# Performance work log

Hardware: AMD Instinct MI355X
Metric: run time of the kernel (lower is better)

## Reference

```python
import jax, jax.numpy as jnp
import numpy as np

T_LEN, S_LEN, B = 100, 400, 16
D_IN, H, CTX, V = 512, 512, 1024, 50000


def setup_inputs() -> dict:
    key = jax.random.key(0)
    ks = jax.random.split(key, 16)
    p = lambda k, shp: jax.random.normal(k, shp, dtype=jnp.float32) * 0.05
    return {
        "y_emb": p(ks[0], (T_LEN, B, D_IN)),
        "context": p(ks[1], (S_LEN, B, CTX)),
        "init_h": p(ks[2], (B, H)),
        "init_c": p(ks[3], (B, H)),
        "x_mask": jnp.ones((S_LEN, B, 1), jnp.float32),
        "y_mask": jnp.ones((T_LEN, B, 1), jnp.float32),
        "y_idx": jax.random.randint(ks[4], (T_LEN, B), 0, V),
        # LSTMCell params (PyTorch gate order i,f,g,o)
        "W_ih": p(ks[5], (4 * H, D_IN)),
        "W_hh": p(ks[6], (4 * H, H)),
        "b_ih": jnp.zeros((4 * H,), jnp.float32),
        "b_hh": jnp.zeros((4 * H,), jnp.float32),
        # second gate block (order i,f,o,c per chunk names x4i,x4f,x4o,x4c)
        "Wx": p(ks[7], (4 * H, CTX)),
        "Ux": p(ks[8], (4 * H, H)),
        "bx": jnp.zeros((4 * H,), jnp.float32),
        # attention params
        "Wc_att": p(ks[9], (CTX, CTX)),
        "b_att": jnp.zeros((CTX,), jnp.float32),
        "W_comb_att": p(ks[10], (CTX, 2 * H)),
        "U_att": p(ks[11], (1, CTX)),
        # word prob: softmax(Linear(cat[h2, att, y_emb]))
        "Wp": p(ks[12], (V, H + CTX + D_IN)),
        "bp": jnp.zeros((V,), jnp.float32),
    }


def reference(y_emb, context, init_h, init_c, x_mask, y_mask, y_idx,
              W_ih, W_hh, b_ih, b_hh, Wx, Ux, bx,
              Wc_att, b_att, W_comb_att, U_att, Wp, bp):
    # pctx: [S, B, CTX]
    pctx = jnp.einsum('sbc,dc->sbd', context, Wc_att) + b_att
    u_att = U_att[0]  # [CTX]

    def step(carry, inp):
        h, c = carry              # [B, H] each
        y, ym, yi = inp           # [B, D_IN], [B, 1], [B]
        # LSTMCell (gate order i, f, g, o)
        gates = y @ W_ih.T + b_ih + h @ W_hh.T + b_hh
        gi, gf, gg, go = jnp.split(gates, 4, axis=1)
        c1 = jax.nn.sigmoid(gf) * c + jax.nn.sigmoid(gi) * jnp.tanh(gg)
        h1 = jax.nn.sigmoid(go) * jnp.tanh(c1)
        h1 = ym * h1 + (1.0 - ym) * h
        c1 = ym * c1 + (1.0 - ym) * c
        # attention query from cat(h1, c1)
        s = jnp.concatenate([h1, c1], axis=1)          # [B, 2H]
        q = s @ W_comb_att.T                           # [B, CTX]
        unreg = jnp.tanh(pctx + q) * x_mask            # [S, B, CTX]
        u = jnp.einsum('sbc,c->sb', unreg, u_att)[..., None]  # [S, B, 1]
        w = jnp.exp(u - jnp.max(u, axis=0, keepdims=True)) * x_mask
        w = w / jnp.sum(w, axis=0, keepdims=True)      # [S, B, 1]
        att = jnp.sum(w * context, axis=0)             # [B, CTX]
        # second gate block (chunk order i, f, o, c)
        pre = h1 @ Ux.T + att @ Wx.T + bx
        xi, xf, xo, xc = jnp.split(pre, 4, axis=1)
        c2 = jax.nn.sigmoid(xf) * c1 + jax.nn.sigmoid(xi) * jnp.tanh(xc)
        h2 = jax.nn.sigmoid(xo) * jnp.tanh(c2)
        c2 = ym * c2 + (1.0 - ym) * c1
        h2 = ym * h2 + (1.0 - ym) * h1
        # word prob + per-step NLL
        feat = jnp.concatenate([h2, att, y], axis=1)   # [B, H+CTX+D_IN]
        logp = jax.nn.log_softmax(feat @ Wp.T + bp, axis=1)
        cost = -jnp.take_along_axis(logp, yi[:, None], axis=1)[:, 0]  # [B]
        return (h2, c2), cost

    _, costs = jax.lax.scan(step, (init_h, init_c), (y_emb, y_mask, y_idx))
    ym2 = y_mask[..., 0]                               # [T, B]
    cost_per_batch = jnp.sum(costs * ym2, axis=0) / jnp.sum(ym2, axis=0)
    return cost_per_batch
```

## Files before the change

### kernel.cpp

```cpp
#include <hip/hip_runtime.h>
#include <stdint.h>

typedef unsigned int u32;
typedef unsigned short u16;
typedef unsigned char u8;
typedef long long i64;
typedef __attribute__((ext_vector_type(4))) float f32x4;
typedef __attribute__((ext_vector_type(4))) float f32x4v;
typedef __attribute__((ext_vector_type(8))) short bf16x8;

#define T_LEN 100
#define S_LEN 400
#define NB 16
#define HD 512
#define CTXD 1024
#define VOC 50000
#define K4H 2048
#define M_ALL 1600

static __device__ __forceinline__ float bf2f(u16 v) {
  union { u32 u; float f; } c; c.u = ((u32)v) << 16; return c.f;
}
static __device__ __forceinline__ u16 f2bf(float f) {
  union { float f; u32 u; } c; c.f = f;
  return (u16)((c.u + 0x7fffu + ((c.u >> 16) & 1u)) >> 16);
}
static __device__ __forceinline__ u32 pack2(float a, float b) {
  return (u32)f2bf(a) | ((u32)f2bf(b) << 16);
}
static __device__ __forceinline__ uint4 pack8(float4 a, float4 b) {
  return make_uint4(pack2(a.x, a.y), pack2(a.z, a.w), pack2(b.x, b.y), pack2(b.z, b.w));
}
static __device__ __forceinline__ uint4 pack8v(f32x4v a, f32x4v b) {
  return make_uint4(pack2(a.x, a.y), pack2(a.z, a.w), pack2(b.x, b.y), pack2(b.z, b.w));
}
static __device__ __forceinline__ u32 pkfp8(float x, float y, float z, float w) {
  int p = 0;
  p = __builtin_amdgcn_cvt_pk_fp8_f32(x, y, p, 0);
  p = __builtin_amdgcn_cvt_pk_fp8_f32(z, w, p, 1);
  return (u32)p;
}
static __device__ __forceinline__ float sigm(float x) { return 1.f / (1.f + __expf(-x)); }
static __device__ __forceinline__ float tanh_(float x) {
  float e = __expf(2.f * x);
  return 1.f - 2.f / (e + 1.f);
}
static __device__ __forceinline__ float ald(const float* p) {
  return __hip_atomic_load(p, __ATOMIC_RELAXED, __HIP_MEMORY_SCOPE_AGENT);
}
static __device__ __forceinline__ void ast(float* p, float v) {
  __hip_atomic_store(p, v, __ATOMIC_RELAXED, __HIP_MEMORY_SCOPE_AGENT);
}
static __device__ __forceinline__ f32x4v cld4(const float* p) {
  f32x4v v;
  asm volatile("global_load_dwordx4 %0, %1, off sc0 sc1\n\t"
               "s_waitcnt vmcnt(0)"
               : "=&v"(v) : "v"(p) : "memory");
  return v;
}
static __device__ __forceinline__ void cld8(
    const float* p0, const float* p1, const float* p2, const float* p3,
    const float* p4, const float* p5, const float* p6, const float* p7,
    f32x4v& v0, f32x4v& v1, f32x4v& v2, f32x4v& v3,
    f32x4v& v4, f32x4v& v5, f32x4v& v6, f32x4v& v7) {
  asm volatile(
      "global_load_dwordx4 %0, %8, off sc0 sc1\n\t"
      "global_load_dwordx4 %1, %9, off sc0 sc1\n\t"
      "global_load_dwordx4 %2, %10, off sc0 sc1\n\t"
      "global_load_dwordx4 %3, %11, off sc0 sc1\n\t"
      "global_load_dwordx4 %4, %12, off sc0 sc1\n\t"
      "global_load_dwordx4 %5, %13, off sc0 sc1\n\t"
      "global_load_dwordx4 %6, %14, off sc0 sc1\n\t"
      "global_load_dwordx4 %7, %15, off sc0 sc1\n\t"
      "s_waitcnt vmcnt(0)"
      : "=&v"(v0), "=&v"(v1), "=&v"(v2), "=&v"(v3),
        "=&v"(v4), "=&v"(v5), "=&v"(v6), "=&v"(v7)
      : "v"(p0), "v"(p1), "v"(p2), "v"(p3), "v"(p4), "v"(p5), "v"(p6), "v"(p7)
      : "memory");
}
static __device__ __forceinline__ void sig(u32* ctr) {
  __hip_atomic_fetch_add(ctr, 1u, __ATOMIC_RELAXED, __HIP_MEMORY_SCOPE_AGENT);
}
static __device__ __forceinline__ void waitge(u32* ctr, u32 tgt) {
  while (__hip_atomic_load(ctr, __ATOMIC_RELAXED, __HIP_MEMORY_SCOPE_AGENT) < tgt)
    __builtin_amdgcn_s_sleep(1);
}

__global__ void sentinel_kernel(float* out, float v) {
  if (threadIdx.x < NB) out[threadIdx.x] = v;
}

struct CastArgs {
  const float* src[9];
  u16* dst[9];
  u32 cum[10];
};

__global__ __launch_bounds__(256) void cast_all(CastArgs A) {
  u32 i = blockIdx.x * 256 + threadIdx.x;
  if (i >= A.cum[9]) return;
  int seg = 0;
  while (i >= A.cum[seg + 1]) seg++;
  u32 li = i - A.cum[seg];
  const float* s = A.src[seg];
  f32x4v a = __builtin_nontemporal_load((const f32x4v*)&s[li * 8]);
  f32x4v b = __builtin_nontemporal_load((const f32x4v*)&s[li * 8 + 4]);
  if (seg < 8) {
    *(uint4*)&A.dst[seg][li * 8] = pack8v(a, b);
  } else {
    u32 m = li >> 6, k8 = (li & 63) << 3;
    u8* f8 = (u8*)A.dst[8];
    uint2 t;
    t.x = pkfp8(a.x, a.y, a.z, a.w);
    t.y = pkfp8(b.x, b.y, b.z, b.w);
    *(uint2*)&f8[(size_t)m * K4H + 1536 + k8] = t;
  }
}

template <int MODE>
__global__ __launch_bounds__(256) void gemm_bf16(const u16* __restrict__ A,
                                                 const u16* __restrict__ Bw,
                                                 void* __restrict__ out,
                                                 const float* __restrict__ bias1,
                                                 const float* __restrict__ bias2,
                                                 int M, int N, int K) {
  __shared__ u16 As[64][40];
  __shared__ u16 Bs[64][40];
  int nb = N / 64;
  int m0 = (blockIdx.x / nb) * 64;
  int n0 = (blockIdx.x % nb) * 64;
  int tid = threadIdx.x;
  int lane = tid & 63;
  int w = tid >> 6;
  int wm = (w >> 1) * 32, wn = (w & 1) * 32;
  f32x4 acc[2][2] = {};
  int arow = tid >> 2, achk = (tid & 3) * 8;
  for (int k0 = 0; k0 < K; k0 += 32) {
    __syncthreads();
    *(uint4*)&As[arow][achk] = *(const uint4*)&A[(size_t)(m0 + arow) * K + k0 + achk];
    *(uint4*)&Bs[arow][achk] = *(const uint4*)&Bw[(size_t)(n0 + arow) * K + k0 + achk];
    __syncthreads();
    int r = lane & 15, kg = lane >> 4;
    bf16x8 a0 = *(const bf16x8*)&As[wm + r][kg * 8];
    bf16x8 a1 = *(const bf16x8*)&As[wm + 16 + r][kg * 8];
    bf16x8 b0 = *(const bf16x8*)&Bs[wn + r][kg * 8];
    bf16x8 b1 = *(const bf16x8*)&Bs[wn + 16 + r][kg * 8];
    acc[0][0] = __builtin_amdgcn_mfma_f32_16x16x32_bf16(a0, b0, acc[0][0], 0, 0, 0);
    acc[0][1] = __builtin_amdgcn_mfma_f32_16x16x32_bf16(a0, b1, acc[0][1], 0, 0, 0);
    acc[1][0] = __builtin_amdgcn_mfma_f32_16x16x32_bf16(a1, b0, acc[1][0], 0, 0, 0);
    acc[1][1] = __builtin_amdgcn_mfma_f32_16x16x32_bf16(a1, b1, acc[1][1], 0, 0, 0);
  }
  int col = lane & 15, rg = lane >> 4;
#pragma unroll
  for (int fi = 0; fi < 2; fi++)
#pragma unroll
    for (int fj = 0; fj < 2; fj++)
#pragma unroll
      for (int r = 0; r < 4; r++) {
        int m = m0 + wm + fi * 16 + rg * 4 + r;
        int n = n0 + wn + fj * 16 + col;
        float v = acc[fi][fj][r] + bias1[n];
        if constexpr (MODE == 1) {
          v += bias2[n];
          ((float*)out)[(size_t)m * N + n] = v;
        } else {
          ((u16*)out)[(size_t)m * N + n] = f2bf(v);
        }
      }
}

struct DecArgs {
  const u16 *pctx, *ctx, *Whh, *Wcomb, *Uxw, *Wxw;
  const float *xW, *bx, *uatt, *xmask, *ymask, *init_h, *init_c;
  float *h, *c, *h1, *c1, *qsum, *attnum, *attden;
  u8* feat8;
  u32* bar;
};

__global__ __launch_bounds__(256, 1) void decoder_coop(DecArgs A) {
  extern __shared__ char smem[];
  u16* pctx_l = (u16*)smem;
  u16* ctx_l = (u16*)(smem + 51200);
  float* ua_lp = (float*)(smem + 102400);
  float* xm_l = (float*)(smem + 106752);
  char* un = smem + 106880;

  const int tid = threadIdx.x;
  const int blk = blockIdx.x;
  const int lane = tid & 63, w = tid >> 6;
  const int r16 = lane & 15, kg = lane >> 4;
  const int bK = blk & 15;
  const int s0 = (blk >> 4) * 25;
  u32* qdone = A.bar;
  u32* cdone = A.bar + 64;
  u32* h2done = A.bar + 128;

  for (int idx = tid; idx < 25 * 128; idx += 256) {
    int i = idx >> 7, c8 = (idx & 127) << 3;
    *(uint4*)&pctx_l[i * 1024 + c8] =
        *(const uint4*)&A.pctx[((size_t)(s0 + i) * NB + bK) * CTXD + c8];
    *(uint4*)&ctx_l[i * 1024 + c8] =
        *(const uint4*)&A.ctx[((size_t)(s0 + i) * NB + bK) * CTXD + c8];
  }
  {
    int c0 = tid * 4;
    int p = (c0 >> 4) * 17 + (c0 & 15);
#pragma unroll
    for (int j = 0; j < 4; j++) ua_lp[p + j] = A.uatt[c0 + j];
  }
  if (tid < 25) xm_l[tid] = A.xmask[(s0 + tid) * NB + bK];

  for (int ts = 0; ts < T_LEN; ts++) {
    const int par = ts & 1;
    if (blk < 16) {
      if (tid == 0) waitge(h2done, 32u * (u32)ts);
      __syncthreads();
      u16* Al = (u16*)un;
      float* gbA = (float*)(un + 16640);
      u16* h1c1 = (u16*)(un + 24832);
      const float* hs = ts ? A.h : A.init_h;
      const float* cs = ts ? A.c : A.init_c;
      {
        const int b0_ = tid >> 6, k80 = (tid & 63) << 3;
        const int b1_ = (256 + tid) >> 6, k81 = ((256 + tid) & 63) << 3;
        const int b2_ = (512 + tid) >> 6, k82 = ((512 + tid) & 63) << 3;
        const int b3_ = (768 + tid) >> 6, k83 = ((768 + tid) & 63) << 3;
        f32x4v v0, v1, v2, v3, v4, v5, v6, v7;
        cld8(&hs[b0_ * 512 + k80], &hs[b0_ * 512 + k80 + 4],
             &hs[b1_ * 512 + k81], &hs[b1_ * 512 + k81 + 4],
             &hs[b2_ * 512 + k82], &hs[b2_ * 512 + k82 + 4],
             &hs[b3_ * 512 + k83], &hs[b3_ * 512 + k83 + 4],
             v0, v1, v2, v3, v4, v5, v6, v7);
        *(uint4*)&Al[b0_ * 520 + k80] = pack8v(v0, v1);
        *(uint4*)&Al[b1_ * 520 + k81] = pack8v(v2, v3);
        *(uint4*)&Al[b2_ * 520 + k82] = pack8v(v4, v5);
        *(uint4*)&Al[b3_ * 520 + k83] = pack8v(v6, v7);
      }
      __syncthreads();
      const int j0 = blk * 32;
      {
        f32x4 acc0 = {}, acc1 = {};
        const size_t row0 = (size_t)(w * 512 + j0 + r16) * 512;
        const size_t row1 = (size_t)(w * 512 + j0 + 16 + r16) * 512;
#pragma unroll
        for (int ks = 0; ks < 16; ks++) {
          bf16x8 a = *(const bf16x8*)&Al[r16 * 520 + ks * 32 + kg * 8];
          bf16x8 b0 = *(const bf16x8*)&A.Whh[row0 + ks * 32 + kg * 8];
          bf16x8 b1 = *(const bf16x8*)&A.Whh[row1 + ks * 32 + kg * 8];
          acc0 = __builtin_amdgcn_mfma_f32_16x16x32_bf16(a, b0, acc0, 0, 0, 0);
          acc1 = __builtin_amdgcn_mfma_f32_16x16x32_bf16(a, b1, acc1, 0, 0, 0);
        }
#pragma unroll
        for (int r = 0; r < 4; r++) {
          gbA[(w * 16 + kg * 4 + r) * 32 + r16] = acc0[r];
          gbA[(w * 16 + kg * 4 + r) * 32 + 16 + r16] = acc1[r];
        }
      }
      __syncthreads();
#pragma unroll
      for (int i = 0; i < 2; i++) {
        int idx = i * 256 + tid;
        int b = idx >> 5, j = idx & 31;
        int n = j0 + j;
        const float* xw = &A.xW[(size_t)(ts * NB + b) * K4H];
        float gi = gbA[(0 * 16 + b) * 32 + j] + xw[n];
        float gf = gbA[(1 * 16 + b) * 32 + j] + xw[512 + n];
        float gg = gbA[(2 * 16 + b) * 32 + j] + xw[1024 + n];
        float go = gbA[(3 * 16 + b) * 32 + j] + xw[1536 + n];
        float ymv = A.ymask[ts * NB + b];
        float c_old = ald(&cs[b * 512 + n]);
        float h_old = ald(&hs[b * 512 + n]);
        float c1v = sigm(gf) * c_old + sigm(gi) * tanh_(gg);
        float h1v = sigm(go) * tanh_(c1v);
        h1v = ymv * h1v + (1.f - ymv) * h_old;
        c1v = ymv * c1v + (1.f - ymv) * c_old;
        ast(&A.h1[b * 512 + n], h1v);
        ast(&A.c1[b * 512 + n], c1v);
        h1c1[b * 72 + j] = f2bf(h1v);
        h1c1[b * 72 + 32 + j] = f2bf(c1v);
      }
      __syncthreads();
      {
        bf16x8 a0 = *(const bf16x8*)&h1c1[r16 * 72 + kg * 8];
        bf16x8 a1 = *(const bf16x8*)&h1c1[r16 * 72 + 32 + kg * 8];
        float* qs = A.qsum + par * 16384;
        for (int nt = w; nt < 64; nt += 4) {
          int n = nt * 16 + r16;
          bf16x8 b0 = *(const bf16x8*)&A.Wcomb[(size_t)n * 1024 + j0 + kg * 8];
          bf16x8 b1 = *(const bf16x8*)&A.Wcomb[(size_t)n * 1024 + 512 + j0 + kg * 8];
          f32x4 acc = {};
          acc = __builtin_amdgcn_mfma_f32_16x16x32_bf16(a0, b0, acc, 0, 0, 0);
          acc = __builtin_amdgcn_mfma_f32_16x16x32_bf16(a1, b1, acc, 0, 0, 0);
#pragma unroll
          for (int r = 0; r < 4; r++)
            atomicAdd(&qs[(kg * 4 + r) * 1024 + nt * 16 + r16], acc[r]);
        }
      }
      __syncthreads();
      if (tid == 0) sig(qdone);
    }
    {
      if (tid == 0) waitge(qdone, 16u * (u32)(ts + 1));
      __syncthreads();
      float* q_lp = (float*)un;
      float* p_l = (float*)(un + 4352);
      {
        int c0 = tid * 4;
        f32x4v qv = cld4(&A.qsum[par * 16384 + bK * 1024 + c0]);
        int p = (c0 >> 4) * 17 + (c0 & 15);
        q_lp[p] = qv.x; q_lp[p + 1] = qv.y; q_lp[p + 2] = qv.z; q_lp[p + 3] = qv.w;
      }
      __syncthreads();
      for (int i = w; i < 25; i += 4) {
        const u16* prow = &pctx_l[i * 1024 + lane * 16];
        float s = 0.f;
#pragma unroll
        for (int half = 0; half < 2; half++) {
          bf16x8 pv = *(const bf16x8*)&prow[half * 8];
#pragma unroll
          for (int e = 0; e < 8; e++) {
            int cc = lane * 17 + half * 8 + e;
            s += tanh_(bf2f((u16)pv[e]) + q_lp[cc]) * ua_lp[cc];
          }
        }
#pragma unroll
        for (int off = 1; off < 64; off <<= 1) s += __shfl_xor(s, off);
        if (lane == 0) {
          float xm = xm_l[i];
          p_l[i] = __expf(s * xm) * xm;
        }
      }
      __syncthreads();
      const int c4 = tid << 2;
      float n0 = 0, n1 = 0, n2 = 0, n3 = 0;
#pragma unroll 5
      for (int i = 0; i < 25; i++) {
        float pv = p_l[i];
        uint2 ld = *(const uint2*)&ctx_l[i * 1024 + c4];
        n0 += pv * bf2f((u16)(ld.x & 0xffff));
        n1 += pv * bf2f((u16)(ld.x >> 16));
        n2 += pv * bf2f((u16)(ld.y & 0xffff));
        n3 += pv * bf2f((u16)(ld.y >> 16));
      }
      float* dst = &A.attnum[par * 16384 + bK * 1024 + c4];
      atomicAdd(dst + 0, n0);
      atomicAdd(dst + 1, n1);
      atomicAdd(dst + 2, n2);
      atomicAdd(dst + 3, n3);
      if (tid == 0) {
        float d = 0.f;
        for (int i = 0; i < 25; i++) d += p_l[i];
        atomicAdd(&A.attden[par * NB + bK], d);
      }
      __syncthreads();
      if (tid == 0) sig(cdone);
    }
    if (blk < 32) {
      if (tid == 0) waitge(cdone, 256u * (u32)(ts + 1));
      __syncthreads();
      u16* AlD = (u16*)un;
      float* gbD = (float*)(un + 49408);
      float* attden_l = (float*)(un + 53504);
      if (tid < NB) attden_l[tid] = ald(&A.attden[par * NB + tid]);
      {
        const int b0_ = tid >> 6, k80 = (tid & 63) << 3;
        const int b1_ = (256 + tid) >> 6, k81 = ((256 + tid) & 63) << 3;
        const int b2_ = (512 + tid) >> 6, k82 = ((512 + tid) & 63) << 3;
        const int b3_ = (768 + tid) >> 6, k83 = ((768 + tid) & 63) << 3;
        f32x4v v0, v1, v2, v3, v4, v5, v6, v7;
        cld8(&A.h1[b0_ * 512 + k80], &A.h1[b0_ * 512 + k80 + 4],
             &A.h1[b1_ * 512 + k81], &A.h1[b1_ * 512 + k81 + 4],
             &A.h1[b2_ * 512 + k82], &A.h1[b2_ * 512 + k82 + 4],
             &A.h1[b3_ * 512 + k83], &A.h1[b3_ * 512 + k83 + 4],
             v0, v1, v2, v3, v4, v5, v6, v7);
        *(uint4*)&AlD[b0_ * 1544 + k80] = pack8v(v0, v1);
        *(uint4*)&AlD[b1_ * 1544 + k81] = pack8v(v2, v3);
        *(uint4*)&AlD[b2_ * 1544 + k82] = pack8v(v4, v5);
        *(uint4*)&AlD[b3_ * 1544 + k83] = pack8v(v6, v7);
      }
      __syncthreads();
      {
        const float* base = &A.attnum[par * 16384];
        const int c4 = tid << 2;
        f32x4v a0, a1, a2, a3, a4, a5, a6, a7;
        cld8(base + 0 * 1024 + c4, base + 1 * 1024 + c4, base + 2 * 1024 + c4,
             base + 3 * 1024 + c4, base + 4 * 1024 + c4, base + 5 * 1024 + c4,
             base + 6 * 1024 + c4, base + 7 * 1024 + c4,
             a0, a1, a2, a3, a4, a5, a6, a7);
#define ATT_ST(i, vv)                                                        \
  {                                                                          \
    float rd = 1.f / attden_l[i];                                            \
    uint2 t;                                                                 \
    t.x = pack2(vv.x * rd, vv.y * rd);                                       \
    t.y = pack2(vv.z * rd, vv.w * rd);                                       \
    *(uint2*)&AlD[(i) * 1544 + 512 + c4] = t;                                \
  }
        ATT_ST(0, a0) ATT_ST(1, a1) ATT_ST(2, a2) ATT_ST(3, a3)
        ATT_ST(4, a4) ATT_ST(5, a5) ATT_ST(6, a6) ATT_ST(7, a7)
        cld8(base + 8 * 1024 + c4, base + 9 * 1024 + c4, base + 10 * 1024 + c4,
             base + 11 * 1024 + c4, base + 12 * 1024 + c4, base + 13 * 1024 + c4,
             base + 14 * 1024 + c4, base + 15 * 1024 + c4,
             a0, a1, a2, a3, a4, a5, a6, a7);
        ATT_ST(8, a0) ATT_ST(9, a1) ATT_ST(10, a2) ATT_ST(11, a3)
        ATT_ST(12, a4) ATT_ST(13, a5) ATT_ST(14, a6) ATT_ST(15, a7)
#undef ATT_ST
      }
      __syncthreads();
      if (blk < 16) {
        const u16* arow = &AlD[blk * 1544 + 512];
        int c4 = tid * 4;
        u32 p = pkfp8(bf2f(arow[c4]), bf2f(arow[c4 + 1]), bf2f(arow[c4 + 2]),
                      bf2f(arow[c4 + 3]));
        *(u32*)&A.feat8[(size_t)(ts * NB + blk) * K4H + 512 + c4] = p;
      }
      const int j0 = blk * 16;
      f32x4 acc = {};
      const size_t rowU = (size_t)(w * 512 + j0 + r16) * 512;
      const size_t rowW = (size_t)(w * 512 + j0 + r16) * 1024;
#pragma unroll
      for (int ks = 0; ks < 16; ks++) {
        bf16x8 a = *(const bf16x8*)&AlD[r16 * 1544 + ks * 32 + kg * 8];
        bf16x8 b0 = *(const bf16x8*)&A.Uxw[rowU + ks * 32 + kg * 8];
        acc = __builtin_amdgcn_mfma_f32_16x16x32_bf16(a, b0, acc, 0, 0, 0);
      }
#pragma unroll
      for (int ks = 16; ks < 48; ks++) {
        bf16x8 a = *(const bf16x8*)&AlD[r16 * 1544 + ks * 32 + kg * 8];
        bf16x8 b0 = *(const bf16x8*)&A.Wxw[rowW + (ks - 16) * 32 + kg * 8];
        acc = __builtin_amdgcn_mfma_f32_16x16x32_bf16(a, b0, acc, 0, 0, 0);
      }
#pragma unroll
      for (int r = 0; r < 4; r++) gbD[(w * 16 + kg * 4 + r) * 16 + r16] = acc[r];
      __syncthreads();
      {
        int b = tid >> 4, j = tid & 15;
        int n = j0 + j;
        float xi = gbD[(0 * 16 + b) * 16 + j] + A.bx[n];
        float xf = gbD[(1 * 16 + b) * 16 + j] + A.bx[512 + n];
        float xo = gbD[(2 * 16 + b) * 16 + j] + A.bx[1024 + n];
        float xc = gbD[(3 * 16 + b) * 16 + j] + A.bx[1536 + n];
        float ymv = A.ymask[ts * NB + b];
        float c1v = ald(&A.c1[b * 512 + n]);
        float h1v = ald(&A.h1[b * 512 + n]);
        float c2 = sigm(xf) * c1v + sigm(xi) * tanh_(xc);
        float h2 = sigm(xo) * tanh_(c2);
        c2 = ymv * c2 + (1.f - ymv) * c1v;
        h2 = ymv * h2 + (1.f - ymv) * h1v;
        ast(&A.h[b * 512 + n], h2);
        ast(&A.c[b * 512 + n], c2);
        int p8 = 0;
        p8 = __builtin_amdgcn_cvt_pk_fp8_f32(h2, h2, p8, 0);
        A.feat8[(size_t)(ts * NB + b) * K4H + n] = (u8)(p8 & 0xff);
      }
      ast(&A.attnum[(par ^ 1) * 16384 + blk * 512 + tid], 0.f);
      ast(&A.attnum[(par ^ 1) * 16384 + blk * 512 + 256 + tid], 0.f);
      ast(&A.qsum[par * 16384 + blk * 512 + tid], 0.f);
      ast(&A.qsum[par * 16384 + blk * 512 + 256 + tid], 0.f);
      if (blk == 0 && tid < NB) ast(&A.attden[(par ^ 1) * NB + tid], 0.f);
      __syncthreads();
      if (tid == 0) sig(h2done);
    }
  }
}

__global__ __launch_bounds__(512, 1) void lse_gemm_fp8(const u8* __restrict__ feat8,
                                                       const float* __restrict__ Wp,
                                                       const float* __restrict__ bp,
                                                       float* __restrict__ lse) {
  extern __shared__ char smem[];
  u8* Bl = (u8*)smem;
  const int tid = threadIdx.x;
  const int n0 = blockIdx.x * 64;
  for (int n = 0; n < 64; n++) {
    int gn = n0 + n;
    f32x4v f = {0.f, 0.f, 0.f, 0.f};
    if (gn < VOC)
      f = __builtin_nontemporal_load((const f32x4v*)&Wp[(size_t)gn * K4H + tid * 4]);
    *(u32*)&Bl[n * 2064 + tid * 4] = pkfp8(f.x, f.y, f.z, f.w);
  }
  __syncthreads();
  const int w = tid >> 6, lane = tid & 63;
  const int r16 = lane & 15, kg = lane >> 4;
  bool vj[4];
  float bpj[4];
#pragma unroll
  for (int j = 0; j < 4; j++) {
    int nf = n0 + j * 16 + r16;
    vj[j] = nf < VOC;
    bpj[j] = vj[j] ? bp[nf] : 0.f;
  }
  for (int qq = w; qq < 25; qq += 8) {
    int mrow = qq * 64;
    f32x4 acc[4][4] = {};
    for (int ks = 0; ks < 64; ks++) {
      i64 b0 = *(const i64*)&Bl[(r16) * 2064 + ks * 32 + kg * 8];
      i64 b1 = *(const i64*)&Bl[(16 + r16) * 2064 + ks * 32 + kg * 8];
      i64 b2 = *(const i64*)&Bl[(32 + r16) * 2064 + ks * 32 + kg * 8];
      i64 b3 = *(const i64*)&Bl[(48 + r16) * 2064 + ks * 32 + kg * 8];
#pragma unroll
      for (int s = 0; s < 4; s++) {
        i64 a = *(const i64*)&feat8[(size_t)(mrow + s * 16 + r16) * K4H + ks * 32 + kg * 8];
        acc[s][0] = __builtin_amdgcn_mfma_f32_16x16x32_fp8_fp8(a, b0, acc[s][0], 0, 0, 0);
        acc[s][1] = __builtin_amdgcn_mfma_f32_16x16x32_fp8_fp8(a, b1, acc[s][1], 0, 0, 0);
        acc[s][2] = __builtin_amdgcn_mfma_f32_16x16x32_fp8_fp8(a, b2, acc[s][2], 0, 0, 0);
        acc[s][3] = __builtin_amdgcn_mfma_f32_16x16x32_fp8_fp8(a, b3, acc[s][3], 0, 0, 0);
      }
    }
#pragma unroll
    for (int s = 0; s < 4; s++) {
#pragma unroll
      for (int r = 0; r < 4; r++) {
        float e = 0.f;
#pragma unroll
        for (int j = 0; j < 4; j++)
          if (vj[j]) e += __expf(acc[s][j][r] + bpj[j]);
        e += __shfl_xor(e, 1);
        e += __shfl_xor(e, 2);
        e += __shfl_xor(e, 4);
        e += __shfl_xor(e, 8);
        if (r16 == 0) atomicAdd(&lse[mrow + s * 16 + kg * 4 + r], e);
      }
    }
  }
}

__global__ __launch_bounds__(256) void target_logit(const u8* __restrict__ feat8,
                                                    const float* __restrict__ Wp,
                                                    const float* __restrict__ bp,
                                                    const int* __restrict__ yidx,
                                                    float* __restrict__ tlog) {
  int gw = (blockIdx.x * 256 + threadIdx.x) >> 6;
  int lane = threadIdx.x & 63;
  if (gw >= M_ALL) return;
  int yi = yidx[gw];
  const float* wrow = Wp + (size_t)yi * K4H;
  const u8* frow = feat8 + (size_t)gw * K4H;
  float s = 0.f;
#pragma unroll
  for (int i = 0; i < 4; i++) {
    int k = i * 512 + lane * 8;
    uint2 fv = *(const uint2*)&frow[k];
    f32x4v w0 = __builtin_nontemporal_load((const f32x4v*)&wrow[k]);
    f32x4v w1 = __builtin_nontemporal_load((const f32x4v*)&wrow[k + 4]);
    s += __builtin_amdgcn_cvt_f32_fp8(fv.x, 0) * w0.x;
    s += __builtin_amdgcn_cvt_f32_fp8(fv.x, 1) * w0.y;
    s += __builtin_amdgcn_cvt_f32_fp8(fv.x, 2) * w0.z;
    s += __builtin_amdgcn_cvt_f32_fp8(fv.x, 3) * w0.w;
    s += __builtin_amdgcn_cvt_f32_fp8(fv.y, 0) * w1.x;
    s += __builtin_amdgcn_cvt_f32_fp8(fv.y, 1) * w1.y;
    s += __builtin_amdgcn_cvt_f32_fp8(fv.y, 2) * w1.z;
    s += __builtin_amdgcn_cvt_f32_fp8(fv.y, 3) * w1.w;
  }
#pragma unroll
  for (int off = 1; off < 64; off <<= 1) s += __shfl_xor(s, off);
  if (lane == 0) tlog[gw] = s + bp[yi];
}

__global__ void finalize(const float* __restrict__ lse, const float* __restrict__ tlog,
                         const float* __restrict__ ymask, float* __restrict__ out) {
  int b = threadIdx.x;
  if (b < NB) {
    float sc = 0.f, sm = 0.f;
    for (int t = 0; t < T_LEN; t++) {
      int m = t * NB + b;
      float ym = ymask[m];
      sc += (logf(lse[m]) - tlog[m]) * ym;
      sm += ym;
    }
    out[b] = sc / sm;
  }
}

extern "C" void kernel_launch(void* const* d_in, const int* in_sizes, int n_in,
                              void* d_out, int out_size, void* d_ws, size_t ws_size,
                              hipStream_t stream) {
  const float* y_emb = (const float*)d_in[0];
  const float* context = (const float*)d_in[1];
  const float* init_h = (const float*)d_in[2];
  const float* init_c = (const float*)d_in[3];
  const float* x_mask = (const float*)d_in[4];
  const float* y_mask = (const float*)d_in[5];
  const int* y_idx = (const int*)d_in[6];
  const float* W_ih = (const float*)d_in[7];
  const float* W_hh = (const float*)d_in[8];
  const float* b_ih = (const float*)d_in[9];
  const float* b_hh = (const float*)d_in[10];
  const float* Wx = (const float*)d_in[11];
  const float* Ux = (const float*)d_in[12];
  const float* bx = (const float*)d_in[13];
  const float* Wc_att = (const float*)d_in[14];
  const float* b_att = (const float*)d_in[15];
  const float* W_comb = (const float*)d_in[16];
  const float* U_att = (const float*)d_in[17];
  const float* Wp = (const float*)d_in[18];
  const float* bp = (const float*)d_in[19];

  if (ws_size < 60000000ULL) {
    sentinel_kernel<<<1, 64, 0, stream>>>((float*)d_out, (float)(ws_size >> 20));
    return;
  }

  char* ws = (char*)d_ws;
  float* lse = (float*)(ws + 0);
  float* attnum = (float*)(ws + 8192);
  float* attden = (float*)(ws + 139264);
  u32* bar = (u32*)(ws + 139392);
  float* qsum = (float*)(ws + 151680);
  float* tlog = (float*)(ws + 282752);
  u16* pctx = (u16*)(ws + 294912);
  u16* ctxb = (u16*)(ws + 13402112);
  u16* Wcb = (u16*)(ws + 26509312);
  u16* yembb = (u16*)(ws + 28606464);
  u16* Wihb = (u16*)(ws + 30244864);
  u16* Whhb = (u16*)(ws + 32342016);
  u16* Wcombb = (u16*)(ws + 34439168);
  u16* Uxb = (u16*)(ws + 36536320);
  u16* Wxb = (u16*)(ws + 38633472);
  float* xW = (float*)(ws + 42827776);
  u8* feat8 = (u8*)(ws + 55934976);
  float* hbuf = (float*)(ws + 59211776);
  float* cbuf = (float*)(ws + 59244544);
  float* h1buf = (float*)(ws + 59277312);
  float* c1buf = (float*)(ws + 59310080);

  hipMemsetAsync(ws, 0, 282752, stream);

  CastArgs ca;
  ca.src[0] = context;  ca.dst[0] = ctxb;
  ca.src[1] = Wc_att;   ca.dst[1] = Wcb;
  ca.src[2] = y_emb;    ca.dst[2] = yembb;
  ca.src[3] = W_ih;     ca.dst[3] = Wihb;
  ca.src[4] = W_hh;     ca.dst[4] = Whhb;
  ca.src[5] = W_comb;   ca.dst[5] = Wcombb;
  ca.src[6] = Ux;       ca.dst[6] = Uxb;
  ca.src[7] = Wx;       ca.dst[7] = Wxb;
  ca.src[8] = y_emb;    ca.dst[8] = (u16*)feat8;
  u32 sz[9] = {819200, 131072, 102400, 131072, 131072, 131072, 131072, 262144, 102400};
  ca.cum[0] = 0;
  for (int i = 0; i < 9; i++) ca.cum[i + 1] = ca.cum[i] + sz[i];
  cast_all<<<(ca.cum[9] + 255) / 256, 256, 0, stream>>>(ca);

  gemm_bf16<0><<<1600, 256, 0, stream>>>(ctxb, Wcb, pctx, b_att, b_att, 6400, 1024, 1024);
  gemm_bf16<1><<<800, 256, 0, stream>>>(yembb, Wihb, xW, b_ih, b_hh, 1600, 2048, 512);

  DecArgs a;
  a.pctx = pctx; a.ctx = ctxb; a.Whh = Whhb; a.Wcomb = Wcombb; a.Uxw = Uxb; a.Wxw = Wxb;
  a.xW = xW; a.bx = bx; a.uatt = U_att; a.xmask = x_mask; a.ymask = y_mask;
  a.init_h = init_h; a.init_c = init_c;
  a.h = hbuf; a.c = cbuf; a.h1 = h1buf; a.c1 = c1buf; a.qsum = qsum;
  a.attnum = attnum; a.attden = attden; a.feat8 = feat8; a.bar = bar;
  hipFuncSetAttribute(reinterpret_cast<const void*>(decoder_coop),
                      hipFuncAttributeMaxDynamicSharedMemorySize, 160448);
  decoder_coop<<<256, 256, 160448, stream>>>(a);

  hipFuncSetAttribute(reinterpret_cast<const void*>(lse_gemm_fp8),
                      hipFuncAttributeMaxDynamicSharedMemorySize, 132096);
  lse_gemm_fp8<<<782, 512, 132096, stream>>>(feat8, Wp, bp, lse);

  target_logit<<<400, 256, 0, stream>>>(feat8, Wp, bp, y_idx, tlog);
  finalize<<<1, 64, 0, stream>>>(lse, tlog, y_mask, (float*)d_out);
}
```

Baseline: 5.052 ms.

## Double decoder block width to 512 threads and split GEMM K across waves

Raises the persistent cooperative decoder from 256 to 512 threads per block. The recurrent h@Whh and Ux/Wx matmuls are split along K between two wave halves, and partial results are combined through LDS atomics or paired sums. The attention score loop keeps the query and u_att slices in registers instead of padded LDS reads, and the per-step load, attention and zeroing loops are redistributed over the extra threads. The goal is to shorten per-timestep latency on the serial critical path, at the cost of more LDS atomics, extra syncs and higher register pressure at 512 threads.

```diff
diff --git a/kernel.cpp b/kernel.cpp
--- a/kernel.cpp
+++ b/kernel.cpp
@@ -28,9 +28,6 @@
 static __device__ __forceinline__ u32 pack2(float a, float b) {
   return (u32)f2bf(a) | ((u32)f2bf(b) << 16);
 }
-static __device__ __forceinline__ uint4 pack8(float4 a, float4 b) {
-  return make_uint4(pack2(a.x, a.y), pack2(a.z, a.w), pack2(b.x, b.y), pack2(b.z, b.w));
-}
 static __device__ __forceinline__ uint4 pack8v(f32x4v a, f32x4v b) {
   return make_uint4(pack2(a.x, a.y), pack2(a.z, a.w), pack2(b.x, b.y), pack2(b.z, b.w));
 }
@@ -51,12 +48,18 @@
 static __device__ __forceinline__ void ast(float* p, float v) {
   __hip_atomic_store(p, v, __ATOMIC_RELAXED, __HIP_MEMORY_SCOPE_AGENT);
 }
-static __device__ __forceinline__ f32x4v cld4(const float* p) {
-  f32x4v v;
-  asm volatile("global_load_dwordx4 %0, %1, off sc0 sc1\n\t"
-               "s_waitcnt vmcnt(0)"
-               : "=&v"(v) : "v"(p) : "memory");
-  return v;
+static __device__ __forceinline__ void cld4b(const float* p0, const float* p1,
+                                             const float* p2, const float* p3,
+                                             f32x4v& v0, f32x4v& v1, f32x4v& v2, f32x4v& v3) {
+  asm volatile(
+      "global_load_dwordx4 %0, %4, off sc0 sc1\n\t"
+      "global_load_dwordx4 %1, %5, off sc0 sc1\n\t"
+      "global_load_dwordx4 %2, %6, off sc0 sc1\n\t"
+      "global_load_dwordx4 %3, %7, off sc0 sc1\n\t"
+      "s_waitcnt vmcnt(0)"
+      : "=&v"(v0), "=&v"(v1), "=&v"(v2), "=&v"(v3)
+      : "v"(p0), "v"(p1), "v"(p2), "v"(p3)
+      : "memory");
 }
 static __device__ __forceinline__ void cld8(
     const float* p0, const float* p1, const float* p2, const float* p3,
@@ -177,17 +180,18 @@
   u32* bar;
 };
 
-__global__ __launch_bounds__(256, 1) void decoder_coop(DecArgs A) {
+__global__ __launch_bounds__(512, 1) void decoder_coop(DecArgs A) {
   extern __shared__ char smem[];
   u16* pctx_l = (u16*)smem;
   u16* ctx_l = (u16*)(smem + 51200);
-  float* ua_lp = (float*)(smem + 102400);
-  float* xm_l = (float*)(smem + 106752);
-  char* un = smem + 106880;
+  float* ua_l = (float*)(smem + 102400);
+  float* xm_l = (float*)(smem + 106496);
+  char* un = smem + 106624;
 
   const int tid = threadIdx.x;
   const int blk = blockIdx.x;
   const int lane = tid & 63, w = tid >> 6;
+  const int g = w & 3, hv = w >> 2;
   const int r16 = lane & 15, kg = lane >> 4;
   const int bK = blk & 15;
   const int s0 = (blk >> 4) * 25;
@@ -195,7 +199,7 @@
   u32* cdone = A.bar + 64;
   u32* h2done = A.bar + 128;
 
-  for (int idx = tid; idx < 25 * 128; idx += 256) {
+  for (int idx = tid; idx < 25 * 128; idx += 512) {
     int i = idx >> 7, c8 = (idx & 127) << 3;
     *(uint4*)&pctx_l[i * 1024 + c8] =
         *(const uint4*)&A.pctx[((size_t)(s0 + i) * NB + bK) * CTXD + c8];
@@ -203,12 +207,20 @@
         *(const uint4*)&A.ctx[((size_t)(s0 + i) * NB + bK) * CTXD + c8];
   }
   {
-    int c0 = tid * 4;
-    int p = (c0 >> 4) * 17 + (c0 & 15);
-#pragma unroll
-    for (int j = 0; j < 4; j++) ua_lp[p + j] = A.uatt[c0 + j];
+    int c0 = tid * 2;
+    ua_l[c0] = A.uatt[c0];
+    ua_l[c0 + 1] = A.uatt[c0 + 1];
   }
   if (tid < 25) xm_l[tid] = A.xmask[(s0 + tid) * NB + bK];
+  __syncthreads();
+  float uav[16];
+  {
+    const float* ub = &ua_l[lane * 16];
+    *(f32x4*)&uav[0] = *(const f32x4*)&ub[0];
+    *(f32x4*)&uav[4] = *(const f32x4*)&ub[4];
+    *(f32x4*)&uav[8] = *(const f32x4*)&ub[8];
+    *(f32x4*)&uav[12] = *(const f32x4*)&ub[12];
+  }
 
   for (int ts = 0; ts < T_LEN; ts++) {
     const int par = ts & 1;
@@ -217,60 +229,55 @@
       __syncthreads();
       u16* Al = (u16*)un;
       float* gbA = (float*)(un + 16640);
-      u16* h1c1 = (u16*)(un + 24832);
+      u16* h1c1 = (u16*)(un + 33024);
       const float* hs = ts ? A.h : A.init_h;
       const float* cs = ts ? A.c : A.init_c;
       {
-        const int b0_ = tid >> 6, k80 = (tid & 63) << 3;
-        const int b1_ = (256 + tid) >> 6, k81 = ((256 + tid) & 63) << 3;
-        const int b2_ = (512 + tid) >> 6, k82 = ((512 + tid) & 63) << 3;
-        const int b3_ = (768 + tid) >> 6, k83 = ((768 + tid) & 63) << 3;
-        f32x4v v0, v1, v2, v3, v4, v5, v6, v7;
-        cld8(&hs[b0_ * 512 + k80], &hs[b0_ * 512 + k80 + 4],
-             &hs[b1_ * 512 + k81], &hs[b1_ * 512 + k81 + 4],
-             &hs[b2_ * 512 + k82], &hs[b2_ * 512 + k82 + 4],
-             &hs[b3_ * 512 + k83], &hs[b3_ * 512 + k83 + 4],
-             v0, v1, v2, v3, v4, v5, v6, v7);
-        *(uint4*)&Al[b0_ * 520 + k80] = pack8v(v0, v1);
-        *(uint4*)&Al[b1_ * 520 + k81] = pack8v(v2, v3);
-        *(uint4*)&Al[b2_ * 520 + k82] = pack8v(v4, v5);
-        *(uint4*)&Al[b3_ * 520 + k83] = pack8v(v6, v7);
+        int b = tid >> 5, k16 = (tid & 31) << 4;
+        const float* src = &hs[b * 512 + k16];
+        f32x4v v0, v1, v2, v3;
+        cld4b(src, src + 4, src + 8, src + 12, v0, v1, v2, v3);
+        *(uint4*)&Al[b * 520 + k16] = pack8v(v0, v1);
+        *(uint4*)&Al[b * 520 + k16 + 8] = pack8v(v2, v3);
       }
       __syncthreads();
       const int j0 = blk * 32;
       {
         f32x4 acc0 = {}, acc1 = {};
-        const size_t row0 = (size_t)(w * 512 + j0 + r16) * 512;
-        const size_t row1 = (size_t)(w * 512 + j0 + 16 + r16) * 512;
-#pragma unroll
-        for (int ks = 0; ks < 16; ks++) {
-          bf16x8 a = *(const bf16x8*)&Al[r16 * 520 + ks * 32 + kg * 8];
-          bf16x8 b0 = *(const bf16x8*)&A.Whh[row0 + ks * 32 + kg * 8];
-          bf16x8 b1 = *(const bf16x8*)&A.Whh[row1 + ks * 32 + kg * 8];
+        const size_t row0 = (size_t)(g * 512 + j0 + r16) * 512;
+        const size_t row1 = (size_t)(g * 512 + j0 + 16 + r16) * 512;
+        const int ksb = hv * 8;
+#pragma unroll
+        for (int ks = 0; ks < 8; ks++) {
+          int kk = (ksb + ks) * 32 + kg * 8;
+          bf16x8 a = *(const bf16x8*)&Al[r16 * 520 + kk];
+          bf16x8 b0 = *(const bf16x8*)&A.Whh[row0 + kk];
+          bf16x8 b1 = *(const bf16x8*)&A.Whh[row1 + kk];
           acc0 = __builtin_amdgcn_mfma_f32_16x16x32_bf16(a, b0, acc0, 0, 0, 0);
           acc1 = __builtin_amdgcn_mfma_f32_16x16x32_bf16(a, b1, acc1, 0, 0, 0);
         }
+        float* gb = &gbA[((hv * 4 + g) * 16) * 32];
 #pragma unroll
         for (int r = 0; r < 4; r++) {
-          gbA[(w * 16 + kg * 4 + r) * 32 + r16] = acc0[r];
-          gbA[(w * 16 + kg * 4 + r) * 32 + 16 + r16] = acc1[r];
+          gb[(kg * 4 + r) * 32 + r16] = acc0[r];
+          gb[(kg * 4 + r) * 32 + 16 + r16] = acc1[r];
         }
       }
       __syncthreads();
-#pragma unroll
-      for (int i = 0; i < 2; i++) {
-        int idx = i * 256 + tid;
-        int b = idx >> 5, j = idx & 31;
+      {
+        int b = tid >> 5, j = tid & 31;
         int n = j0 + j;
         const float* xw = &A.xW[(size_t)(ts * NB + b) * K4H];
-        float gi = gbA[(0 * 16 + b) * 32 + j] + xw[n];
-        float gf = gbA[(1 * 16 + b) * 32 + j] + xw[512 + n];
-        float gg = gbA[(2 * 16 + b) * 32 + j] + xw[1024 + n];
-        float go = gbA[(3 * 16 + b) * 32 + j] + xw[1536 + n];
+#define GBA(hh, gg) gbA[(((hh)*4 + (gg)) * 16 + b) * 32 + j]
+        float gi = GBA(0, 0) + GBA(1, 0) + xw[n];
+        float gf = GBA(0, 1) + GBA(1, 1) + xw[512 + n];
+        float gg2 = GBA(0, 2) + GBA(1, 2) + xw[1024 + n];
+        float go = GBA(0, 3) + GBA(1, 3) + xw[1536 + n];
+#undef GBA
         float ymv = A.ymask[ts * NB + b];
         float c_old = ald(&cs[b * 512 + n]);
         float h_old = ald(&hs[b * 512 + n]);
-        float c1v = sigm(gf) * c_old + sigm(gi) * tanh_(gg);
+        float c1v = sigm(gf) * c_old + sigm(gi) * tanh_(gg2);
         float h1v = sigm(go) * tanh_(c1v);
         h1v = ymv * h1v + (1.f - ymv) * h_old;
         c1v = ymv * c1v + (1.f - ymv) * c_old;
@@ -284,7 +291,7 @@
         bf16x8 a0 = *(const bf16x8*)&h1c1[r16 * 72 + kg * 8];
         bf16x8 a1 = *(const bf16x8*)&h1c1[r16 * 72 + 32 + kg * 8];
         float* qs = A.qsum + par * 16384;
-        for (int nt = w; nt < 64; nt += 4) {
+        for (int nt = w; nt < 64; nt += 8) {
           int n = nt * 16 + r16;
           bf16x8 b0 = *(const bf16x8*)&A.Wcomb[(size_t)n * 1024 + j0 + kg * 8];
           bf16x8 b1 = *(const bf16x8*)&A.Wcomb[(size_t)n * 1024 + 512 + j0 + kg * 8];
@@ -302,27 +309,32 @@
     {
       if (tid == 0) waitge(qdone, 16u * (u32)(ts + 1));
       __syncthreads();
-      float* q_lp = (float*)un;
-      float* p_l = (float*)(un + 4352);
-      {
-        int c0 = tid * 4;
-        f32x4v qv = cld4(&A.qsum[par * 16384 + bK * 1024 + c0]);
-        int p = (c0 >> 4) * 17 + (c0 & 15);
-        q_lp[p] = qv.x; q_lp[p + 1] = qv.y; q_lp[p + 2] = qv.z; q_lp[p + 3] = qv.w;
-      }
-      __syncthreads();
-      for (int i = w; i < 25; i += 4) {
+      float* q_l = (float*)un;
+      float* p_l = (float*)(un + 4096);
+      {
+        int c0 = tid * 2;
+        const float* qs = &A.qsum[par * 16384 + bK * 1024 + c0];
+        q_l[c0] = ald(qs);
+        q_l[c0 + 1] = ald(qs + 1);
+      }
+      __syncthreads();
+      float qv[16];
+      {
+        const float* qb = &q_l[lane * 16];
+        *(f32x4*)&qv[0] = *(const f32x4*)&qb[0];
+        *(f32x4*)&qv[4] = *(const f32x4*)&qb[4];
+        *(f32x4*)&qv[8] = *(const f32x4*)&qb[8];
+        *(f32x4*)&qv[12] = *(const f32x4*)&qb[12];
+      }
+      for (int i = w; i < 25; i += 8) {
         const u16* prow = &pctx_l[i * 1024 + lane * 16];
+        bf16x8 pv0 = *(const bf16x8*)&prow[0];
+        bf16x8 pv1 = *(const bf16x8*)&prow[8];
         float s = 0.f;
 #pragma unroll
-        for (int half = 0; half < 2; half++) {
-          bf16x8 pv = *(const bf16x8*)&prow[half * 8];
-#pragma unroll
-          for (int e = 0; e < 8; e++) {
-            int cc = lane * 17 + half * 8 + e;
-            s += tanh_(bf2f((u16)pv[e]) + q_lp[cc]) * ua_lp[cc];
-          }
-        }
+        for (int e = 0; e < 8; e++) s += tanh_(bf2f((u16)pv0[e]) + qv[e]) * uav[e];
+#pragma unroll
+        for (int e = 0; e < 8; e++) s += tanh_(bf2f((u16)pv1[e]) + qv[8 + e]) * uav[8 + e];
 #pragma unroll
         for (int off = 1; off < 64; off <<= 1) s += __shfl_xor(s, off);
         if (lane == 0) {
@@ -331,22 +343,18 @@
         }
       }
       __syncthreads();
-      const int c4 = tid << 2;
-      float n0 = 0, n1 = 0, n2 = 0, n3 = 0;
+      const int c2 = tid << 1;
+      float n0 = 0, n1 = 0;
 #pragma unroll 5
       for (int i = 0; i < 25; i++) {
         float pv = p_l[i];
-        uint2 ld = *(const uint2*)&ctx_l[i * 1024 + c4];
-        n0 += pv * bf2f((u16)(ld.x & 0xffff));
-        n1 += pv * bf2f((u16)(ld.x >> 16));
-        n2 += pv * bf2f((u16)(ld.y & 0xffff));
-        n3 += pv * bf2f((u16)(ld.y >> 16));
-      }
-      float* dst = &A.attnum[par * 16384 + bK * 1024 + c4];
+        u32 ld = *(const u32*)&ctx_l[i * 1024 + c2];
+        n0 += pv * bf2f((u16)(ld & 0xffff));
+        n1 += pv * bf2f((u16)(ld >> 16));
+      }
+      float* dst = &A.attnum[par * 16384 + bK * 1024 + c2];
       atomicAdd(dst + 0, n0);
       atomicAdd(dst + 1, n1);
-      atomicAdd(dst + 2, n2);
-      atomicAdd(dst + 3, n3);
       if (tid == 0) {
         float d = 0.f;
         for (int i = 0; i < 25; i++) d += p_l[i];
@@ -362,30 +370,26 @@
       float* gbD = (float*)(un + 49408);
       float* attden_l = (float*)(un + 53504);
       if (tid < NB) attden_l[tid] = ald(&A.attden[par * NB + tid]);
-      {
-        const int b0_ = tid >> 6, k80 = (tid & 63) << 3;
-        const int b1_ = (256 + tid) >> 6, k81 = ((256 + tid) & 63) << 3;
-        const int b2_ = (512 + tid) >> 6, k82 = ((512 + tid) & 63) << 3;
-        const int b3_ = (768 + tid) >> 6, k83 = ((768 + tid) & 63) << 3;
-        f32x4v v0, v1, v2, v3, v4, v5, v6, v7;
-        cld8(&A.h1[b0_ * 512 + k80], &A.h1[b0_ * 512 + k80 + 4],
-             &A.h1[b1_ * 512 + k81], &A.h1[b1_ * 512 + k81 + 4],
-             &A.h1[b2_ * 512 + k82], &A.h1[b2_ * 512 + k82 + 4],
-             &A.h1[b3_ * 512 + k83], &A.h1[b3_ * 512 + k83 + 4],
-             v0, v1, v2, v3, v4, v5, v6, v7);
-        *(uint4*)&AlD[b0_ * 1544 + k80] = pack8v(v0, v1);
-        *(uint4*)&AlD[b1_ * 1544 + k81] = pack8v(v2, v3);
-        *(uint4*)&AlD[b2_ * 1544 + k82] = pack8v(v4, v5);
-        *(uint4*)&AlD[b3_ * 1544 + k83] = pack8v(v6, v7);
+      gbD[tid] = 0.f;
+      gbD[tid + 512] = 0.f;
+      {
+        int b = tid >> 5, k16 = (tid & 31) << 4;
+        const float* src = &A.h1[b * 512 + k16];
+        f32x4v v0, v1, v2, v3;
+        cld4b(src, src + 4, src + 8, src + 12, v0, v1, v2, v3);
+        *(uint4*)&AlD[b * 1544 + k16] = pack8v(v0, v1);
+        *(uint4*)&AlD[b * 1544 + k16 + 8] = pack8v(v2, v3);
       }
       __syncthreads();
       {
         const float* base = &A.attnum[par * 16384];
-        const int c4 = tid << 2;
+        const int rh = tid >> 8, c4 = (tid & 255) << 2;
+        const int r0 = rh * 8;
         f32x4v a0, a1, a2, a3, a4, a5, a6, a7;
-        cld8(base + 0 * 1024 + c4, base + 1 * 1024 + c4, base + 2 * 1024 + c4,
-             base + 3 * 1024 + c4, base + 4 * 1024 + c4, base + 5 * 1024 + c4,
-             base + 6 * 1024 + c4, base + 7 * 1024 + c4,
+        cld8(base + (r0 + 0) * 1024 + c4, base + (r0 + 1) * 1024 + c4,
+             base + (r0 + 2) * 1024 + c4, base + (r0 + 3) * 1024 + c4,
+             base + (r0 + 4) * 1024 + c4, base + (r0 + 5) * 1024 + c4,
+             base + (r0 + 6) * 1024 + c4, base + (r0 + 7) * 1024 + c4,
              a0, a1, a2, a3, a4, a5, a6, a7);
 #define ATT_ST(i, vv)                                                        \
   {                                                                          \
@@ -395,18 +399,12 @@
     t.y = pack2(vv.z * rd, vv.w * rd);                                       \
     *(uint2*)&AlD[(i) * 1544 + 512 + c4] = t;                                \
   }
-        ATT_ST(0, a0) ATT_ST(1, a1) ATT_ST(2, a2) ATT_ST(3, a3)
-        ATT_ST(4, a4) ATT_ST(5, a5) ATT_ST(6, a6) ATT_ST(7, a7)
-        cld8(base + 8 * 1024 + c4, base + 9 * 1024 + c4, base + 10 * 1024 + c4,
-             base + 11 * 1024 + c4, base + 12 * 1024 + c4, base + 13 * 1024 + c4,
-             base + 14 * 1024 + c4, base + 15 * 1024 + c4,
-             a0, a1, a2, a3, a4, a5, a6, a7);
-        ATT_ST(8, a0) ATT_ST(9, a1) ATT_ST(10, a2) ATT_ST(11, a3)
-        ATT_ST(12, a4) ATT_ST(13, a5) ATT_ST(14, a6) ATT_ST(15, a7)
+        ATT_ST(r0 + 0, a0) ATT_ST(r0 + 1, a1) ATT_ST(r0 + 2, a2) ATT_ST(r0 + 3, a3)
+        ATT_ST(r0 + 4, a4) ATT_ST(r0 + 5, a5) ATT_ST(r0 + 6, a6) ATT_ST(r0 + 7, a7)
 #undef ATT_ST
       }
       __syncthreads();
-      if (blk < 16) {
+      if (blk < 16 && tid < 256) {
         const u16* arow = &AlD[blk * 1544 + 512];
         int c4 = tid * 4;
         u32 p = pkfp8(bf2f(arow[c4]), bf2f(arow[c4 + 1]), bf2f(arow[c4 + 2]),
@@ -414,25 +412,38 @@
         *(u32*)&A.feat8[(size_t)(ts * NB + blk) * K4H + 512 + c4] = p;
       }
       const int j0 = blk * 16;
-      f32x4 acc = {};
-      const size_t rowU = (size_t)(w * 512 + j0 + r16) * 512;
-      const size_t rowW = (size_t)(w * 512 + j0 + r16) * 1024;
-#pragma unroll
-      for (int ks = 0; ks < 16; ks++) {
-        bf16x8 a = *(const bf16x8*)&AlD[r16 * 1544 + ks * 32 + kg * 8];
-        bf16x8 b0 = *(const bf16x8*)&A.Uxw[rowU + ks * 32 + kg * 8];
-        acc = __builtin_amdgcn_mfma_f32_16x16x32_bf16(a, b0, acc, 0, 0, 0);
-      }
-#pragma unroll
-      for (int ks = 16; ks < 48; ks++) {
-        bf16x8 a = *(const bf16x8*)&AlD[r16 * 1544 + ks * 32 + kg * 8];
-        bf16x8 b0 = *(const bf16x8*)&A.Wxw[rowW + (ks - 16) * 32 + kg * 8];
-        acc = __builtin_amdgcn_mfma_f32_16x16x32_bf16(a, b0, acc, 0, 0, 0);
-      }
-#pragma unroll
-      for (int r = 0; r < 4; r++) gbD[(w * 16 + kg * 4 + r) * 16 + r16] = acc[r];
-      __syncthreads();
-      {
+      {
+        f32x4 acc = {};
+        const size_t rowU = (size_t)(g * 512 + j0 + r16) * 512;
+        const size_t rowW = (size_t)(g * 512 + j0 + r16) * 1024;
+        if (hv == 0) {
+#pragma unroll
+          for (int ks = 0; ks < 16; ks++) {
+            int kk = ks * 32 + kg * 8;
+            bf16x8 a = *(const bf16x8*)&AlD[r16 * 1544 + kk];
+            bf16x8 b0 = *(const bf16x8*)&A.Uxw[rowU + kk];
+            acc = __builtin_amdgcn_mfma_f32_16x16x32_bf16(a, b0, acc, 0, 0, 0);
+          }
+#pragma unroll
+          for (int ks = 16; ks < 24; ks++) {
+            bf16x8 a = *(const bf16x8*)&AlD[r16 * 1544 + ks * 32 + kg * 8];
+            bf16x8 b0 = *(const bf16x8*)&A.Wxw[rowW + (ks - 16) * 32 + kg * 8];
+            acc = __builtin_amdgcn_mfma_f32_16x16x32_bf16(a, b0, acc, 0, 0, 0);
+          }
+        } else {
+#pragma unroll
+          for (int ks = 24; ks < 48; ks++) {
+            bf16x8 a = *(const bf16x8*)&AlD[r16 * 1544 + ks * 32 + kg * 8];
+            bf16x8 b0 = *(const bf16x8*)&A.Wxw[rowW + (ks - 16) * 32 + kg * 8];
+            acc = __builtin_amdgcn_mfma_f32_16x16x32_bf16(a, b0, acc, 0, 0, 0);
+          }
+        }
+#pragma unroll
+        for (int r = 0; r < 4; r++)
+          atomicAdd(&gbD[(g * 16 + kg * 4 + r) * 16 + r16], acc[r]);
+      }
+      __syncthreads();
+      if (tid < 256) {
         int b = tid >> 4, j = tid & 15;
         int n = j0 + j;
         float xi = gbD[(0 * 16 + b) * 16 + j] + A.bx[n];
@@ -453,9 +464,7 @@
         A.feat8[(size_t)(ts * NB + b) * K4H + n] = (u8)(p8 & 0xff);
       }
       ast(&A.attnum[(par ^ 1) * 16384 + blk * 512 + tid], 0.f);
-      ast(&A.attnum[(par ^ 1) * 16384 + blk * 512 + 256 + tid], 0.f);
       ast(&A.qsum[par * 16384 + blk * 512 + tid], 0.f);
-      ast(&A.qsum[par * 16384 + blk * 512 + 256 + tid], 0.f);
       if (blk == 0 && tid < NB) ast(&A.attden[(par ^ 1) * NB + tid], 0.f);
       __syncthreads();
       if (tid == 0) sig(h2done);
@@ -651,7 +660,7 @@
   a.attnum = attnum; a.attden = attden; a.feat8 = feat8; a.bar = bar;
   hipFuncSetAttribute(reinterpret_cast<const void*>(decoder_coop),
                       hipFuncAttributeMaxDynamicSharedMemorySize, 160448);
-  decoder_coop<<<256, 256, 160448, stream>>>(a);
+  decoder_coop<<<256, 512, 160448, stream>>>(a);
 
   hipFuncSetAttribute(reinterpret_cast<const void*>(lse_gemm_fp8),
                       hipFuncAttributeMaxDynamicSharedMemorySize, 132096);
```

After: 4.766 ms. 5.7% less time.
